# Performance work log

Hardware: AMD Instinct MI355X
Metric: run time of the kernel (lower is better)

Reference implementation:

```python
import jax, jax.numpy as jnp
import numpy as np

N_STREAMS = 4
DIM = 1024  # per-stream channels C
SINKHORN_ITERS = 50
SINKHORN_TAU = 0.1
RMS_EPS = 1.1920929e-07  # torch.finfo(float32).eps (nn.RMSNorm default eps=None)


def setup_inputs() -> dict:
    key = jax.random.key(0)
    ks = jax.random.split(key, 6)
    B, T = 4, 2048
    n, C = N_STREAMS, DIM
    wd = n * C  # widened_dim
    x = jax.random.normal(ks[0], (B, T, wd), dtype=jnp.float32)
    # projection weights, init std=0.01 (stored as [out, in] like nn.Linear)
    W_res = 0.01 * jax.random.normal(ks[1], (n * n, wd), dtype=jnp.float32)
    W_pre = 0.01 * jax.random.normal(ks[2], (n, wd), dtype=jnp.float32)
    W_post = 0.01 * jax.random.normal(ks[3], (n, wd), dtype=jnp.float32)
    # base logits
    H_res_base = jnp.full((n, n), -0.5, dtype=jnp.float32)
    H_res_base = H_res_base.at[jnp.arange(n), jnp.arange(n)].set(0.0)
    H_pre_base = jnp.zeros((n,), dtype=jnp.float32).at[0].set(1.0)
    H_post_base = jnp.zeros((n,), dtype=jnp.float32)
    gate = jnp.array([5.0], dtype=jnp.float32)
    # branch_fn stand-in: single C->C linear
    W_branch = (1.0 / np.sqrt(C)) * jax.random.normal(ks[4], (C, C), dtype=jnp.float32)
    return {"x": x, "W_res": W_res, "W_pre": W_pre, "W_post": W_post,
            "H_res_base": H_res_base, "H_pre_base": H_pre_base,
            "H_post_base": H_post_base, "gate": gate, "W_branch": W_branch}


def sinkhorn_log(logits, num_iters=SINKHORN_ITERS, tau=SINKHORN_TAU):
    # logits: [..., n, n]
    Z = logits / tau
    u0 = jnp.zeros(Z.shape[:-1], Z.dtype)  # [..., n]
    v0 = jnp.zeros_like(u0)

    def step(carry, _):
        u, v = carry
        u = -jax.nn.logsumexp(Z + v[..., None, :], axis=-1)
        v = -jax.nn.logsumexp(Z + u[..., :, None], axis=-2)
        return (u, v), None

    (u, v), _ = jax.lax.scan(step, (u0, v0), None, length=num_iters)
    return jnp.exp(Z + u[..., :, None] + v[..., None, :])


def reference(x, W_res, W_pre, W_post, H_res_base, H_pre_base, H_post_base, gate, W_branch):
    B, T, nC = x.shape
    n = N_STREAMS
    C = nC // n
    # RMSNorm (no affine)
    x_norm = x * jax.lax.rsqrt(jnp.mean(x * x, axis=-1, keepdims=True) + RMS_EPS)
    # projections (Linear stores [out, in])
    H_res_logits = (x_norm @ W_res.T).reshape(B, T, n, n) + H_res_base
    H_pre_logits = x_norm @ W_pre.T + H_pre_base
    H_post_logits = x_norm @ W_post.T + H_post_base
    H_res = sinkhorn_log(H_res_logits)
    H_pre = jax.nn.softmax(H_pre_logits, axis=-1)
    H_post = jax.nn.softmax(H_post_logits, axis=-1)
    g = jax.nn.sigmoid(gate)[0]  # eval mode: no exploration noise
    I = jnp.eye(n, dtype=H_res.dtype)
    H_res = (1.0 - g) * I + g * H_res
    x_streams = x.reshape(B, T, n, C)
    x_pre = jnp.einsum('btnc,btn->btc', x_streams, H_pre)
    y = x_pre @ W_branch  # branch_fn stand-in
    x_mixed = jnp.einsum('btij,btjc->btic', H_res, x_streams)
    y_distributed = jnp.einsum('btc,btn->btnc', y, H_post)
    return (x_mixed + y_distributed).reshape(B, T, nC)
```

## Files before the change

kernel.cpp:

```cpp
#include <hip/hip_runtime.h>
#include <cstdint>
#include <cstddef>

#define NTOK 8192
#define WD   4096
#define CD   1024
#define EPS_RMS 1.1920929e-07f
#define TAU_INV 10.0f

using half8  = __attribute__((ext_vector_type(8))) _Float16;
using half4v = __attribute__((ext_vector_type(4))) _Float16;
using f32x4  = __attribute__((ext_vector_type(4))) float;

__global__ __launch_bounds__(256) void k_prep(const float* __restrict__ W,
                                              _Float16* __restrict__ WT,
                                              const float* __restrict__ Wres,
                                              const float* __restrict__ Wpre,
                                              const float* __restrict__ Wpost,
                                              _Float16* __restrict__ Wcat) {
  if (blockIdx.x < 256) {
    __shared__ float tile[64][65];
    const int t  = threadIdx.x;
    const int c0 = (blockIdx.x & 15) * 64;
    const int k0 = (blockIdx.x >> 4) * 64;
    const int a = t & 63, b = t >> 6;
#pragma unroll
    for (int i = 0; i < 16; ++i) {
      int k = b + i * 4;
      tile[k][a] = W[(size_t)(k0 + k) * CD + (c0 + a)];
    }
    __syncthreads();
#pragma unroll
    for (int i = 0; i < 16; ++i) {
      int c = b + i * 4;
      WT[(size_t)(c0 + c) * CD + (k0 + a)] = (_Float16)tile[a][c];
    }
  } else {
    const int id  = (blockIdx.x - 256) * 256 + threadIdx.x;
    const int row = id >> 10;
    const int kq  = id & 1023;
    float4 v = make_float4(0.f, 0.f, 0.f, 0.f);
    if (row < 16)      v = *(const float4*)(Wres + (size_t)row * WD + kq * 4);
    else if (row < 20) v = *(const float4*)(Wpre + (size_t)(row - 16) * WD + kq * 4);
    else if (row < 24) v = *(const float4*)(Wpost + (size_t)(row - 20) * WD + kq * 4);
    half4v h;
    h[0] = (_Float16)v.x; h[1] = (_Float16)v.y; h[2] = (_Float16)v.z; h[3] = (_Float16)v.w;
    *(half4v*)(Wcat + (size_t)row * WD + kq * 4) = h;
  }
}

#define KCH 512
__global__ __launch_bounds__(512, 6) void k_stats4(
    const float* __restrict__ x, const _Float16* __restrict__ Wcat,
    const float* __restrict__ baseRes, const float* __restrict__ basePre,
    const float* __restrict__ basePost, const float* __restrict__ gate,
    float* __restrict__ HpostOut, float* __restrict__ HresF,
    _Float16* __restrict__ xpre)
{
  __shared__ float Lpart[8][16][32];
  __shared__ float ssPart[8][16];
  __shared__ float invS[16];
  __shared__ float HpreS[16][4];

  const int t    = threadIdx.x;
  const int lane = t & 63;
  const int p    = t >> 6;
  const int tok0 = blockIdx.x * 16;
  const int fr   = lane & 15, kg = lane >> 4;

  const float*    xr = x    + (size_t)(tok0 + fr) * WD + p * KCH + kg * 8;
  const _Float16* w0 = Wcat + (size_t)fr * WD        + p * KCH + kg * 8;
  const _Float16* w1 = Wcat + (size_t)(16 + fr) * WD + p * KCH + kg * 8;

  f32x4 acc0 = {0.f, 0.f, 0.f, 0.f};
  f32x4 acc1 = {0.f, 0.f, 0.f, 0.f};
  float ss = 0.f;

#pragma unroll
  for (int kt = 0; kt < 16; ++kt) {
    const int ko = kt * 32;
    const float4 u = *(const float4*)(xr + ko);
    const float4 v = *(const float4*)(xr + ko + 4);
    const half8 b0 = *(const half8*)(w0 + ko);
    const half8 b1 = *(const half8*)(w1 + ko);
    ss += u.x * u.x + u.y * u.y + u.z * u.z + u.w * u.w;
    ss += v.x * v.x + v.y * v.y + v.z * v.z + v.w * v.w;
    half8 a;
    a[0] = (_Float16)u.x; a[1] = (_Float16)u.y; a[2] = (_Float16)u.z; a[3] = (_Float16)u.w;
    a[4] = (_Float16)v.x; a[5] = (_Float16)v.y; a[6] = (_Float16)v.z; a[7] = (_Float16)v.w;
    acc0 = __builtin_amdgcn_mfma_f32_16x16x32_f16(a, b0, acc0, 0, 0, 0);
    acc1 = __builtin_amdgcn_mfma_f32_16x16x32_f16(a, b1, acc1, 0, 0, 0);
  }

  ss += __shfl_xor(ss, 16);
  ss += __shfl_xor(ss, 32);
  if (lane < 16) ssPart[p][lane] = ss;

#pragma unroll
  for (int r = 0; r < 4; ++r) {
    Lpart[p][kg * 4 + r][fr]      = acc0[r];
    Lpart[p][kg * 4 + r][16 + fr] = acc1[r];
  }
  __syncthreads();

  if (t < 16) {
    float s = 0.f;
#pragma unroll
    for (int pp = 0; pp < 8; ++pp) s += ssPart[pp][t];
    const float inv = rsqrtf(s * (1.0f / (float)WD) + EPS_RMS);
    invS[t] = inv;
    float pr[4], q[4];
#pragma unroll
    for (int j = 0; j < 4; ++j) {
      float lp = 0.f, lq = 0.f;
#pragma unroll
      for (int pp = 0; pp < 8; ++pp) {
        lp += Lpart[pp][t][16 + j];
        lq += Lpart[pp][t][20 + j];
      }
      pr[j] = fmaf(lp, inv, basePre[j]);
      q[j]  = fmaf(lq, inv, basePost[j]);
    }
    {
      const float m = fmaxf(fmaxf(pr[0], pr[1]), fmaxf(pr[2], pr[3]));
      float s2 = 0.f;
#pragma unroll
      for (int j = 0; j < 4; ++j) { pr[j] = __expf(pr[j] - m); s2 += pr[j]; }
      const float rs = 1.0f / s2;
#pragma unroll
      for (int j = 0; j < 4; ++j) HpreS[t][j] = pr[j] * rs;
    }
    {
      const float m = fmaxf(fmaxf(q[0], q[1]), fmaxf(q[2], q[3]));
      float s2 = 0.f;
#pragma unroll
      for (int j = 0; j < 4; ++j) { q[j] = __expf(q[j] - m); s2 += q[j]; }
      const float rs = 1.0f / s2;
      float4 qv; qv.x = q[0] * rs; qv.y = q[1] * rs; qv.z = q[2] * rs; qv.w = q[3] * rs;
      *(float4*)(HpostOut + (size_t)(tok0 + t) * 4) = qv;
    }
  }
  __syncthreads();

  if (t < 256) {
    const int tk  = t >> 4;
    const int l16 = t & 15;
    float Lsum = 0.f;
#pragma unroll
    for (int pp = 0; pp < 8; ++pp) Lsum += Lpart[pp][tk][l16];
    const float Z = fmaf(Lsum, invS[tk], baseRes[l16]) * TAU_INV;
    const int i = l16 >> 2, j = l16 & 3;
    float u = 0.0f, v = 0.0f;
    for (int itr = 0; itr < 50; ++itr) {
      float a = Z + v;
      float m = fmaxf(a, __shfl_xor(a, 1)); m = fmaxf(m, __shfl_xor(m, 2));
      float s = __expf(a - m);
      s += __shfl_xor(s, 1); s += __shfl_xor(s, 2);
      u = -(m + __logf(s));
      float b = Z + u;
      float m2 = fmaxf(b, __shfl_xor(b, 4)); m2 = fmaxf(m2, __shfl_xor(m2, 8));
      float s2 = __expf(b - m2);
      s2 += __shfl_xor(s2, 4); s2 += __shfl_xor(s2, 8);
      v = -(m2 + __logf(s2));
    }
    const float H = __expf(Z + u + v);
    const float gg = 1.0f / (1.0f + __expf(-gate[0]));
    HresF[(size_t)(tok0 + tk) * 16 + l16] = gg * H + ((i == j) ? (1.0f - gg) : 0.0f);
  } else {
    const int q16 = (t - 256) >> 4;
    const int l16 = t & 15;
    const int tok = tok0 + q16;
    const float p0 = HpreS[q16][0], p1 = HpreS[q16][1];
    const float p2 = HpreS[q16][2], p3 = HpreS[q16][3];
    const float* xrow = x + (size_t)tok * WD;
    _Float16* xp = xpre + (size_t)tok * CD;
#pragma unroll 2
    for (int it = 0; it < 16; ++it) {
      const int c4 = it * 64 + l16 * 4;
      const float4 s0 = *(const float4*)(xrow + c4);
      const float4 s1 = *(const float4*)(xrow + CD + c4);
      const float4 s2 = *(const float4*)(xrow + 2 * CD + c4);
      const float4 s3 = *(const float4*)(xrow + 3 * CD + c4);
      half4v h;
      h[0] = (_Float16)(p0 * s0.x + p1 * s1.x + p2 * s2.x + p3 * s3.x);
      h[1] = (_Float16)(p0 * s0.y + p1 * s1.y + p2 * s2.y + p3 * s3.y);
      h[2] = (_Float16)(p0 * s0.z + p1 * s1.z + p2 * s2.z + p3 * s3.z);
      h[3] = (_Float16)(p0 * s0.w + p1 * s1.w + p2 * s2.w + p3 * s3.w);
      *(half4v*)(xp + c4) = h;
    }
  }
}

#define LDK 72
__global__ __launch_bounds__(256, 4) void k_gemm_epi(
    const _Float16* __restrict__ xpre, const _Float16* __restrict__ WT,
    const float* __restrict__ x, const float* __restrict__ HresF,
    const float* __restrict__ Hpost, float* __restrict__ out)
{
  __shared__ _Float16 As[64 * LDK];
  __shared__ _Float16 Bs[128 * LDK];
  const int tid  = threadIdx.x;
  const int nb   = blockIdx.x & 7;
  const int mb   = blockIdx.x >> 3;
  const int tok0 = mb * 64;
  const int cb   = nb * 128;
  const int lane = tid & 63, wid = tid >> 6;
  const int wc   = wid * 32;
  const int fr = lane & 15, kg = lane >> 4;

  f32x4 acc[4][2];
#pragma unroll
  for (int m = 0; m < 4; ++m)
#pragma unroll
    for (int n = 0; n < 2; ++n) { f32x4 z = {0.f, 0.f, 0.f, 0.f}; acc[m][n] = z; }

  for (int kt = 0; kt < 16; ++kt) {
#pragma unroll
    for (int i = 0; i < 2; ++i) {
      const int chunk = tid + i * 256;
      const int r = chunk >> 3;
      const int ko = (chunk & 7) * 8;
      *(half8*)&As[r * LDK + ko] =
          *(const half8*)&xpre[(size_t)(tok0 + r) * CD + kt * 64 + ko];
    }
#pragma unroll
    for (int i = 0; i < 4; ++i) {
      const int chunk = tid + i * 256;
      const int r = chunk >> 3;
      const int ko = (chunk & 7) * 8;
      *(half8*)&Bs[r * LDK + ko] =
          *(const half8*)&WT[(size_t)(cb + r) * CD + kt * 64 + ko];
    }
    __syncthreads();
#pragma unroll
    for (int kk = 0; kk < 2; ++kk) {
      half8 a[4], b[2];
#pragma unroll
      for (int m = 0; m < 4; ++m)
        a[m] = *(const half8*)&As[(m * 16 + fr) * LDK + kk * 32 + kg * 8];
#pragma unroll
      for (int n = 0; n < 2; ++n)
        b[n] = *(const half8*)&Bs[(wc + n * 16 + fr) * LDK + kk * 32 + kg * 8];
#pragma unroll
      for (int m = 0; m < 4; ++m)
#pragma unroll
        for (int n = 0; n < 2; ++n)
          acc[m][n] = __builtin_amdgcn_mfma_f32_16x16x32_f16(a[m], b[n], acc[m][n], 0, 0, 0);
    }
    __syncthreads();
  }

  float* Hs = (float*)As;
  for (int idx = tid; idx < 64 * 20; idx += 256) {
    const int tl = idx / 20, e = idx % 20;
    Hs[idx] = (e < 16) ? HresF[(size_t)(tok0 + tl) * 16 + e]
                       : Hpost[(size_t)(tok0 + tl) * 4 + (e - 16)];
  }
  __syncthreads();

#pragma unroll
  for (int m = 0; m < 4; ++m) {
#pragma unroll
    for (int reg = 0; reg < 4; ++reg) {
      const int tl = m * 16 + kg * 4 + reg;
      const size_t trow = (size_t)(tok0 + tl) * WD;
      float H[20];
#pragma unroll
      for (int e = 0; e < 20; ++e) H[e] = Hs[tl * 20 + e];
#pragma unroll
      for (int n = 0; n < 2; ++n) {
        const int c = cb + wc + n * 16 + fr;
        const float yv = acc[m][n][reg];
        const float x0 = x[trow + c];
        const float x1 = x[trow + CD + c];
        const float x2 = x[trow + 2 * CD + c];
        const float x3 = x[trow + 3 * CD + c];
#pragma unroll
        for (int i = 0; i < 4; ++i) {
          out[trow + i * CD + c] =
              H[i * 4 + 0] * x0 + H[i * 4 + 1] * x1 + H[i * 4 + 2] * x2 +
              H[i * 4 + 3] * x3 + H[16 + i] * yv;
        }
      }
    }
  }
}

extern "C" void kernel_launch(void* const* d_in, const int* in_sizes, int n_in,
                              void* d_out, int out_size, void* d_ws, size_t ws_size,
                              hipStream_t stream) {
  const float* x        = (const float*)d_in[0];
  const float* Wres     = (const float*)d_in[1];
  const float* Wpre     = (const float*)d_in[2];
  const float* Wpost    = (const float*)d_in[3];
  const float* baseRes  = (const float*)d_in[4];
  const float* basePre  = (const float*)d_in[5];
  const float* basePost = (const float*)d_in[6];
  const float* gate     = (const float*)d_in[7];
  const float* Wb       = (const float*)d_in[8];
  float* out = (float*)d_out;

  char* ws = (char*)d_ws;
  _Float16* xpre  = (_Float16*)(ws);
  _Float16* WT    = (_Float16*)(ws + 16777216);
  float*    HresF = (float*)(ws + 19398656);
  float*    Hpst  = (float*)(ws + 19922944);
  _Float16* Wcat  = (_Float16*)(ws + 20054016);

  k_prep<<<384, 256, 0, stream>>>(Wb, WT, Wres, Wpre, Wpost, Wcat);
  k_stats4<<<512, 512, 0, stream>>>(x, Wcat, baseRes, basePre, basePost, gate,
                                    Hpst, HresF, xpre);
  k_gemm_epi<<<1024, 256, 0, stream>>>(xpre, WT, x, HresF, Hpst, out);
}
```

Measured before the change: 142.5 us.

## Register-prefetch GEMM tiles and stage epilogue through LDS for float4 I/O

```diff
diff --git a/kernel.cpp b/kernel.cpp
--- a/kernel.cpp
+++ b/kernel.cpp
@@ -192,13 +192,16 @@
 }
 
 #define LDK 72
+#define SMEM_BYTES 38912
 __global__ __launch_bounds__(256, 4) void k_gemm_epi(
     const _Float16* __restrict__ xpre, const _Float16* __restrict__ WT,
     const float* __restrict__ x, const float* __restrict__ HresF,
     const float* __restrict__ Hpost, float* __restrict__ out)
 {
-  __shared__ _Float16 As[64 * LDK];
-  __shared__ _Float16 Bs[128 * LDK];
+  __shared__ __align__(16) char smem[SMEM_BYTES];
+  _Float16* As = (_Float16*)smem;
+  _Float16* Bs = (_Float16*)(smem + 9216);
+
   const int tid  = threadIdx.x;
   const int nb   = blockIdx.x & 7;
   const int mb   = blockIdx.x >> 3;
@@ -208,49 +211,71 @@
   const int wc   = wid * 32;
   const int fr = lane & 15, kg = lane >> 4;
 
+  const int sr = tid >> 3;
+  const int sk = (tid & 7) * 8;
+  const _Float16* pA = xpre + (size_t)(tok0 + sr) * CD + sk;
+  const _Float16* pB = WT   + (size_t)(cb  + sr) * CD + sk;
+
   f32x4 acc[4][2];
 #pragma unroll
   for (int m = 0; m < 4; ++m)
 #pragma unroll
     for (int n = 0; n < 2; ++n) { f32x4 z = {0.f, 0.f, 0.f, 0.f}; acc[m][n] = z; }
 
+  half8 a0 = *(const half8*)(pA);
+  half8 a1 = *(const half8*)(pA + 32 * CD);
+  half8 b0 = *(const half8*)(pB);
+  half8 b1 = *(const half8*)(pB + 32 * CD);
+  half8 b2 = *(const half8*)(pB + 64 * CD);
+  half8 b3 = *(const half8*)(pB + 96 * CD);
+
   for (int kt = 0; kt < 16; ++kt) {
-#pragma unroll
-    for (int i = 0; i < 2; ++i) {
-      const int chunk = tid + i * 256;
-      const int r = chunk >> 3;
-      const int ko = (chunk & 7) * 8;
-      *(half8*)&As[r * LDK + ko] =
-          *(const half8*)&xpre[(size_t)(tok0 + r) * CD + kt * 64 + ko];
-    }
-#pragma unroll
-    for (int i = 0; i < 4; ++i) {
-      const int chunk = tid + i * 256;
-      const int r = chunk >> 3;
-      const int ko = (chunk & 7) * 8;
-      *(half8*)&Bs[r * LDK + ko] =
-          *(const half8*)&WT[(size_t)(cb + r) * CD + kt * 64 + ko];
-    }
     __syncthreads();
+    *(half8*)&As[sr * LDK + sk]        = a0;
+    *(half8*)&As[(sr + 32) * LDK + sk] = a1;
+    *(half8*)&Bs[sr * LDK + sk]        = b0;
+    *(half8*)&Bs[(sr + 32) * LDK + sk] = b1;
+    *(half8*)&Bs[(sr + 64) * LDK + sk] = b2;
+    *(half8*)&Bs[(sr + 96) * LDK + sk] = b3;
+    if (kt < 15) {
+      const int ko = (kt + 1) * 64;
+      a0 = *(const half8*)(pA + ko);
+      a1 = *(const half8*)(pA + 32 * CD + ko);
+      b0 = *(const half8*)(pB + ko);
+      b1 = *(const half8*)(pB + 32 * CD + ko);
+      b2 = *(const half8*)(pB + 64 * CD + ko);
+      b3 = *(const half8*)(pB + 96 * CD + ko);
+    }
+    __syncthreads();
 #pragma unroll
     for (int kk = 0; kk < 2; ++kk) {
-      half8 a[4], b[2];
+      half8 af[4], bf[2];
 #pragma unroll
       for (int m = 0; m < 4; ++m)
-        a[m] = *(const half8*)&As[(m * 16 + fr) * LDK + kk * 32 + kg * 8];
+        af[m] = *(const half8*)&As[(m * 16 + fr) * LDK + kk * 32 + kg * 8];
 #pragma unroll
       for (int n = 0; n < 2; ++n)
-        b[n] = *(const half8*)&Bs[(wc + n * 16 + fr) * LDK + kk * 32 + kg * 8];
+        bf[n] = *(const half8*)&Bs[(wc + n * 16 + fr) * LDK + kk * 32 + kg * 8];
 #pragma unroll
       for (int m = 0; m < 4; ++m)
 #pragma unroll
         for (int n = 0; n < 2; ++n)
-          acc[m][n] = __builtin_amdgcn_mfma_f32_16x16x32_f16(a[m], b[n], acc[m][n], 0, 0, 0);
-    }
-    __syncthreads();
-  }
-
-  float* Hs = (float*)As;
+          acc[m][n] = __builtin_amdgcn_mfma_f32_16x16x32_f16(af[m], bf[n], acc[m][n], 0, 0, 0);
+    }
+  }
+  __syncthreads();
+
+  float* yl = (float*)smem;
+  float* Hs = (float*)(smem + 33792);
+#pragma unroll
+  for (int m = 0; m < 4; ++m)
+#pragma unroll
+    for (int reg = 0; reg < 4; ++reg) {
+      const int tl = m * 16 + kg * 4 + reg;
+#pragma unroll
+      for (int n = 0; n < 2; ++n)
+        yl[tl * 132 + wc + n * 16 + fr] = acc[m][n][reg];
+    }
   for (int idx = tid; idx < 64 * 20; idx += 256) {
     const int tl = idx / 20, e = idx % 20;
     Hs[idx] = (e < 16) ? HresF[(size_t)(tok0 + tl) * 16 + e]
@@ -258,30 +283,29 @@
   }
   __syncthreads();
 
-#pragma unroll
-  for (int m = 0; m < 4; ++m) {
-#pragma unroll
-    for (int reg = 0; reg < 4; ++reg) {
-      const int tl = m * 16 + kg * 4 + reg;
-      const size_t trow = (size_t)(tok0 + tl) * WD;
-      float H[20];
-#pragma unroll
-      for (int e = 0; e < 20; ++e) H[e] = Hs[tl * 20 + e];
-#pragma unroll
-      for (int n = 0; n < 2; ++n) {
-        const int c = cb + wc + n * 16 + fr;
-        const float yv = acc[m][n][reg];
-        const float x0 = x[trow + c];
-        const float x1 = x[trow + CD + c];
-        const float x2 = x[trow + 2 * CD + c];
-        const float x3 = x[trow + 3 * CD + c];
-#pragma unroll
-        for (int i = 0; i < 4; ++i) {
-          out[trow + i * CD + c] =
-              H[i * 4 + 0] * x0 + H[i * 4 + 1] * x1 + H[i * 4 + 2] * x2 +
-              H[i * 4 + 3] * x3 + H[16 + i] * yv;
-        }
-      }
+#pragma unroll 2
+  for (int it = 0; it < 8; ++it) {
+    const int idx = it * 256 + tid;
+    const int tl  = idx >> 5;
+    const int cq  = (idx & 31) * 4;
+    const int c   = cb + cq;
+    const size_t trow = (size_t)(tok0 + tl) * WD;
+    const float4 yv = *(const float4*)&yl[tl * 132 + cq];
+    const float4 x0 = *(const float4*)(x + trow + c);
+    const float4 x1 = *(const float4*)(x + trow + CD + c);
+    const float4 x2 = *(const float4*)(x + trow + 2 * CD + c);
+    const float4 x3 = *(const float4*)(x + trow + 3 * CD + c);
+    const float* H = &Hs[tl * 20];
+#pragma unroll
+    for (int i = 0; i < 4; ++i) {
+      const float h0 = H[i * 4 + 0], h1 = H[i * 4 + 1];
+      const float h2 = H[i * 4 + 2], h3 = H[i * 4 + 3], hy = H[16 + i];
+      float4 o;
+      o.x = h0 * x0.x + h1 * x1.x + h2 * x2.x + h3 * x3.x + hy * yv.x;
+      o.y = h0 * x0.y + h1 * x1.y + h2 * x2.y + h3 * x3.y + hy * yv.y;
+      o.z = h0 * x0.z + h1 * x1.z + h2 * x2.z + h3 * x3.z + hy * yv.z;
+      o.w = h0 * x0.w + h1 * x1.w + h2 * x2.w + h3 * x3.w + hy * yv.w;
+      *(float4*)(out + trow + i * CD + c) = o;
     }
   }
 }
```

Result: slower. 146.6 us (+2.9%).
